# Kernel tuning notes

Hardware: AMD Instinct MI355X
Metric: run time of the kernel (lower is better)

Reference implementation:

```python
import jax, jax.numpy as jnp
import numpy as np

NUM_GRAPHS = 1024  # number of graphs in the batch (readout segments)


def setup_inputs() -> dict:
    key = jax.random.key(0)
    ks = jax.random.split(key, 10)
    N, F_IN, F1, F2, E = 100000, 64, 128, 64, 3200000
    x = jax.random.normal(ks[0], (N, F_IN), dtype=jnp.float32)
    adj = jax.random.randint(ks[1], (2, E), 0, N, dtype=jnp.int64)
    batch = jnp.sort(jax.random.randint(ks[2], (N,), 0, NUM_GRAPHS, dtype=jnp.int64))
    def xavier(k, shape):
        fan_in, fan_out = shape
        lim = jnp.sqrt(6.0 / (fan_in + fan_out))
        return jax.random.uniform(k, shape, jnp.float32, -lim, lim)
    W1 = xavier(ks[3], (F_IN, F1)); b1 = jax.random.uniform(ks[4], (F1,), jnp.float32)
    W2 = xavier(ks[5], (F1, F2));  b2 = jax.random.uniform(ks[6], (F2,), jnp.float32)
    Wm = xavier(ks[7], (2 * F2, F2)); bm = jax.random.uniform(ks[8], (F2,), jnp.float32)
    return {"x": x, "adj": adj, "batch": batch,
            "W1": W1, "b1": b1, "W2": W2, "b2": b2, "Wm": Wm, "bm": bm}


def _gcn_conv(x, W, b, src, dst):
    # GCNConv: out = D^{-1/2} (A + I) D^{-1/2} X W + b
    N = x.shape[0]
    h = x @ W  # [N, F_out]
    loops = jnp.arange(N, dtype=src.dtype)
    src_a = jnp.concatenate([src, loops])  # add self-loops
    dst_a = jnp.concatenate([dst, loops])
    deg = jax.ops.segment_sum(jnp.ones(src_a.shape[0], h.dtype), dst_a, num_segments=N)
    dinv = jax.lax.rsqrt(deg)  # deg >= 1 due to self-loops
    norm = dinv[src_a] * dinv[dst_a]  # [E+N]
    msg = h[src_a] * norm[:, None]    # gather + scale (memory-bound)
    return jax.ops.segment_sum(msg, dst_a, num_segments=N) + b


def _readout_meanmax(x, batch):
    G = NUM_GRAPHS
    s = jax.ops.segment_sum(x, batch, num_segments=G)
    cnt = jax.ops.segment_sum(jnp.ones(x.shape[0], x.dtype), batch, num_segments=G)
    mean = s / jnp.maximum(cnt, 1.0)[:, None]
    mx = jax.ops.segment_max(x, batch, num_segments=G)
    return jnp.concatenate([mean, mx], axis=1)  # [G, 2*F2]


def reference(x, adj, batch, W1, b1, W2, b2, Wm, bm):
    src, dst = adj[0], adj[1]
    h = jax.nn.relu(_gcn_conv(x, W1, b1, src, dst))
    h = _gcn_conv(h, W2, b2, src, dst)
    r = _readout_meanmax(h, batch)
    return r @ Wm + bm
```

## Files before the change

kernel.cpp:

```cpp
#include <hip/hip_runtime.h>
#include <hip/hip_fp16.h>
#include <cstdint>
#include <cstddef>

#define NGRAPH 1024
#define CHUNK 8192
#define SCTHREADS 512
#define SCIT (CHUNK / SCTHREADS)
#define MAXB 512
#define CAP 16384

typedef _Float16 f16x8 __attribute__((ext_vector_type(8)));
typedef float f32x4 __attribute__((ext_vector_type(4)));


__global__ __launch_bounds__(SCTHREADS) void scatter1_kernel(const int* __restrict__ src,
        const int* __restrict__ dst, int E, int B,
        int* __restrict__ bcnt, unsigned* __restrict__ ebuck) {
    __shared__ unsigned sorted[CHUNK];
    __shared__ int h[MAXB];
    __shared__ int lo[MAXB];
    __shared__ int cur[MAXB];
    __shared__ int gbase[MAXB];
    int blk = blockIdx.x, tid = threadIdx.x;
    int base = blk * CHUNK;
    int cnt_i = E - base; if (cnt_i > CHUNK) cnt_i = CHUNK;

    h[tid] = 0;
    __syncthreads();

    unsigned rd[SCIT], rs[SCIT];
    #pragma unroll
    for (int it = 0; it < SCIT; ++it) {
        int i = base + tid + it * SCTHREADS;
        if (i < E) {
            rd[it] = (unsigned)dst[i];
            rs[it] = (unsigned)src[i];
            atomicAdd(&h[rd[it] >> 8], 1);
        } else rd[it] = 0xFFFFFFFFu;
    }
    __syncthreads();

    int hv = h[tid];
    if (tid < B) gbase[tid] = hv ? atomicAdd(&bcnt[tid], hv) : 0;

    for (int o = 1; o < SCTHREADS; o <<= 1) {
        int t = (tid >= o) ? h[tid - o] : 0;
        __syncthreads();
        h[tid] += t;
        __syncthreads();
    }
    int excl = h[tid] - hv;
    lo[tid] = excl;
    cur[tid] = excl;
    __syncthreads();

    #pragma unroll
    for (int it = 0; it < SCIT; ++it) {
        if (rd[it] != 0xFFFFFFFFu) {
            int b = rd[it] >> 8;
            int p = atomicAdd(&cur[b], 1);
            sorted[p] = ((rd[it] & 255u) << 24) | rs[it];
        }
    }
    __syncthreads();

    for (int j = tid; j < cnt_i; j += SCTHREADS) {
        int l = (int)(((long long)j * B) / cnt_i);
        if (l > B - 1) l = B - 1;
        while (lo[l] > j) --l;
        while (l + 1 < B && lo[l + 1] <= j) ++l;
        ebuck[(size_t)l * CAP + gbase[l] + (j - lo[l])] = sorted[j];
    }
}

__global__ __launch_bounds__(256) void fine_kernel(const unsigned* __restrict__ ebuck,
        const int* __restrict__ bcnt, const float* __restrict__ x, int N, int B,
        int* __restrict__ row_beg, int* __restrict__ row_end, float* __restrict__ dinv,
        int* __restrict__ esrc, __half* __restrict__ xs) {
    __shared__ int hcnt[256];
    __shared__ int sc[256];
    __shared__ int loff[256];
    __shared__ float sdinv[256];
    int b = blockIdx.x, tid = threadIdx.x;
    int beg = b * CAP;
    int cnt = bcnt[b];
    hcnt[tid] = 0;
    __syncthreads();
    for (int e = tid; e < cnt; e += 256)
        atomicAdd(&hcnt[ebuck[beg + e] >> 24], 1);
    __syncthreads();
    int v = hcnt[tid];
    sc[tid] = v; __syncthreads();
    for (int o = 1; o < 256; o <<= 1) {
        int t = (tid >= o) ? sc[tid - o] : 0;
        __syncthreads();
        sc[tid] += t;
        __syncthreads();
    }
    int excl = sc[tid] - v;
    int n = (b << 8) + tid;
    float d = rsqrtf((float)(v + 1));
    if (n < N) {
        row_beg[n] = beg + excl;
        row_end[n] = beg + excl + v;
        dinv[n] = d;
    }
    loff[tid] = excl;
    sdinv[tid] = d;
    __syncthreads();
    for (int e = tid; e < cnt; e += 256) {
        unsigned u = ebuck[beg + e];
        int p = atomicAdd(&loff[u >> 24], 1);
        esrc[beg + p] = (int)(u & 0xFFFFFF);
    }
    const float4* xr = (const float4*)x;
    #pragma unroll
    for (int it = 0; it < 16; ++it) {
        int j = tid + it * 256;
        int node = j >> 4, cc = j & 15;
        int gn = (b << 8) + node;
        if (gn < N) {
            float dd = sdinv[node];
            float4 vv = xr[(size_t)gn * 16 + cc];
            __half2 h0 = __floats2half2_rn(vv.x * dd, vv.y * dd);
            __half2 h1 = __floats2half2_rn(vv.z * dd, vv.w * dd);
            uint2 u;
            u.x = *(unsigned*)&h0;
            u.y = *(unsigned*)&h1;
            ((uint2*)xs)[(size_t)gn * 16 + cc] = u;
        }
    }
}

__global__ __launch_bounds__(256) void prep_kernel(const float* __restrict__ W1,
        const float* __restrict__ W2, __half* __restrict__ W1s, __half* __restrict__ W2s,
        const int* __restrict__ batch, int N, int* __restrict__ goff,
        int* __restrict__ bcnt) {
    int t = threadIdx.x;
    if (blockIdx.x == 0) {
        #pragma unroll
        for (int it = 0; it < 4; ++it) {
            int s = t + it * 256;
            int n = s & 15, q = (s >> 4) & 3, nt = (s >> 6) & 7, ks = s >> 9;
            int k0 = ks * 32 + q * 8, col = nt * 16 + n;
            __align__(16) __half h[8];
            #pragma unroll
            for (int j = 0; j < 8; ++j) h[j] = (__half)W1[(k0 + j) * 128 + col];
            *((uint4*)&W1s[(size_t)s * 8]) = *(uint4*)h;
        }
        #pragma unroll
        for (int it = 0; it < 4; ++it) {
            int s = t + it * 256;
            int n = s & 15, q = (s >> 4) & 3, n2 = (s >> 6) & 3, ks2 = s >> 8;
            int k0 = ks2 * 32 + q * 8, col = n2 * 16 + n;
            __align__(16) __half h[8];
            #pragma unroll
            for (int j = 0; j < 8; ++j) h[j] = (__half)W2[(k0 + j) * 64 + col];
            *((uint4*)&W2s[(size_t)s * 8]) = *(uint4*)h;
        }
    } else {
        int g = (blockIdx.x - 1) * 256 + t;
        if (g < MAXB) bcnt[g] = 0;
        if (g > NGRAPH) return;
        if (g == NGRAPH) { goff[g] = N; return; }
        int lo = 0, hi = N;
        while (lo < hi) {
            int mid = (lo + hi) >> 1;
            if (batch[mid] < g) lo = mid + 1; else hi = mid;
        }
        goff[g] = lo;
    }
}

__device__ inline void acc8h(__half2* a, const uint4& u) {
    const __half2* h = (const __half2*)&u;
    #pragma unroll
    for (int i = 0; i < 4; ++i) a[i] = __hadd2(a[i], h[i]);
}

__global__ __launch_bounds__(256) void agg_h2h_kernel(const __half* __restrict__ xs,
        const int* __restrict__ esrc, const int* __restrict__ row_beg,
        const int* __restrict__ row_end, const float* __restrict__ dinv,
        __half* __restrict__ out, int N) {
    int n = blockIdx.x * 4 + (threadIdx.x >> 6);
    if (n >= N) return;
    int lane = threadIdx.x & 63;
    int g = lane >> 3, c = lane & 7;
    const uint4* xs4 = (const uint4*)xs;
    int beg = row_beg[n], end = row_end[n];
    __half2 ha[4] = {}, hb[4] = {};
    if (g == 0) acc8h(ha, xs4[(size_t)n * 8 + c]);
    int e = beg + g;
    for (; e + 8 < end; e += 16) {
        int s0 = esrc[e], s1 = esrc[e + 8];
        uint4 u0 = xs4[(size_t)s0 * 8 + c];
        uint4 u1 = xs4[(size_t)s1 * 8 + c];
        acc8h(ha, u0);
        acc8h(hb, u1);
    }
    if (e < end) acc8h(ha, xs4[(size_t)esrc[e] * 8 + c]);
    float a[8];
    #pragma unroll
    for (int i = 0; i < 4; ++i) {
        float2 fa = __half22float2(ha[i]), fb = __half22float2(hb[i]);
        a[2 * i]     = fa.x + fb.x;
        a[2 * i + 1] = fa.y + fb.y;
    }
    #pragma unroll
    for (int i = 0; i < 8; ++i) {
        a[i] += __shfl_xor(a[i], 8, 64);
        a[i] += __shfl_xor(a[i], 16, 64);
        a[i] += __shfl_xor(a[i], 32, 64);
    }
    if (g == 0) {
        float d = dinv[n];
        __align__(16) __half2 h[4];
        #pragma unroll
        for (int i = 0; i < 4; ++i)
            h[i] = __floats2half2_rn(a[2 * i] * d, a[2 * i + 1] * d);
        ((uint4*)out)[(size_t)n * 8 + c] = *(uint4*)h;
    }
}

__global__ __launch_bounds__(256) void agg_h2f_kernel(const __half* __restrict__ xs,
        const int* __restrict__ esrc, const int* __restrict__ row_beg,
        const int* __restrict__ row_end, const float* __restrict__ dinv,
        const float* __restrict__ bias, float* __restrict__ out, int N) {
    int n = blockIdx.x * 4 + (threadIdx.x >> 6);
    if (n >= N) return;
    int lane = threadIdx.x & 63;
    int g = lane >> 3, c = lane & 7;
    const uint4* xs4 = (const uint4*)xs;
    int beg = row_beg[n], end = row_end[n];
    __half2 ha[4] = {}, hb[4] = {};
    if (g == 0) acc8h(ha, xs4[(size_t)n * 8 + c]);
    int e = beg + g;
    for (; e + 8 < end; e += 16) {
        int s0 = esrc[e], s1 = esrc[e + 8];
        uint4 u0 = xs4[(size_t)s0 * 8 + c];
        uint4 u1 = xs4[(size_t)s1 * 8 + c];
        acc8h(ha, u0);
        acc8h(hb, u1);
    }
    if (e < end) acc8h(ha, xs4[(size_t)esrc[e] * 8 + c]);
    float a[8];
    #pragma unroll
    for (int i = 0; i < 4; ++i) {
        float2 fa = __half22float2(ha[i]), fb = __half22float2(hb[i]);
        a[2 * i]     = fa.x + fb.x;
        a[2 * i + 1] = fa.y + fb.y;
    }
    #pragma unroll
    for (int i = 0; i < 8; ++i) {
        a[i] += __shfl_xor(a[i], 8, 64);
        a[i] += __shfl_xor(a[i], 16, 64);
        a[i] += __shfl_xor(a[i], 32, 64);
    }
    if (g == 0) {
        float d = dinv[n];
        float4 bb0 = ((const float4*)bias)[c * 2];
        float4 bb1 = ((const float4*)bias)[c * 2 + 1];
        float4 o0, o1;
        o0.x = a[0] * d + bb0.x; o0.y = a[1] * d + bb0.y;
        o0.z = a[2] * d + bb0.z; o0.w = a[3] * d + bb0.w;
        o1.x = a[4] * d + bb1.x; o1.y = a[5] * d + bb1.y;
        o1.z = a[6] * d + bb1.z; o1.w = a[7] * d + bb1.w;
        ((float4*)out)[(size_t)n * 16 + c * 2] = o0;
        ((float4*)out)[(size_t)n * 16 + c * 2 + 1] = o1;
    }
}

__global__ __launch_bounds__(256) void fusedmlp_kernel(const __half* __restrict__ A,
        const __half* __restrict__ W1s, const __half* __restrict__ W2s,
        const float* __restrict__ b1, const float* __restrict__ dinv,
        __half* __restrict__ T, int N) {
    __shared__ __align__(16) __half h1t[4][16][136];
    int tid = threadIdx.x;
    int w = tid >> 6, lane = tid & 63;
    int n15 = lane & 15, q = lane >> 4;
    int base = blockIdx.x * 64 + w * 16;

    int m = base + n15; if (m >= N) m = N - 1;
    const uint4* Ar = (const uint4*)(A + (size_t)m * 64);
    uint4 ua0 = Ar[q];
    uint4 ua1 = Ar[4 + q];
    f16x8 a10 = *(f16x8*)&ua0;
    f16x8 a11 = *(f16x8*)&ua1;
    const uint4* W1f = (const uint4*)W1s;
    #pragma unroll
    for (int nt = 0; nt < 8; ++nt) {
        f32x4 c = {0.f, 0.f, 0.f, 0.f};
        uint4 ub0 = W1f[(nt * 4 + q) * 16 + n15];
        uint4 ub1 = W1f[((8 + nt) * 4 + q) * 16 + n15];
        c = __builtin_amdgcn_mfma_f32_16x16x32_f16(a10, *(f16x8*)&ub0, c, 0, 0, 0);
        c = __builtin_amdgcn_mfma_f32_16x16x32_f16(a11, *(f16x8*)&ub1, c, 0, 0, 0);
        float bv = b1[nt * 16 + n15];
        #pragma unroll
        for (int rr = 0; rr < 4; ++rr) {
            float hv = fmaxf(c[rr] + bv, 0.f);
            h1t[w][q * 4 + rr][nt * 16 + n15] = (__half)hv;
        }
    }
    __syncthreads();

    f16x8 a2[4];
    #pragma unroll
    for (int ks2 = 0; ks2 < 4; ++ks2)
        a2[ks2] = *(f16x8*)&h1t[w][n15][ks2 * 32 + q * 8];
    const uint4* W2f = (const uint4*)W2s;
    #pragma unroll
    for (int n2 = 0; n2 < 4; ++n2) {
        f32x4 c = {0.f, 0.f, 0.f, 0.f};
        #pragma unroll
        for (int ks2 = 0; ks2 < 4; ++ks2) {
            uint4 ub = W2f[((ks2 * 4 + n2) * 4 + q) * 16 + n15];
            c = __builtin_amdgcn_mfma_f32_16x16x32_f16(a2[ks2], *(f16x8*)&ub, c, 0, 0, 0);
        }
        #pragma unroll
        for (int rr = 0; rr < 4; ++rr) {
            int node = base + q * 4 + rr;
            if (node < N) {
                float v = c[rr] * dinv[node];
                T[(size_t)node * 64 + n2 * 16 + n15] = (__half)v;
            }
        }
    }
}

__global__ __launch_bounds__(256) void readout_head_kernel(const float* __restrict__ h2,
        const int* __restrict__ goff, const float* __restrict__ Wm,
        const float* __restrict__ bm, float* __restrict__ out) {
    int g = blockIdx.x;
    int beg = goff[g], end = goff[g + 1];
    int f = threadIdx.x & 63;
    int c = threadIdx.x >> 6;
    float s = 0.f, m = -3.4e38f;
    for (int n = beg + c; n < end; n += 4) {
        float v = h2[(size_t)n * 64 + f];
        s += v;
        m = fmaxf(m, v);
    }
    __shared__ float ss[4][64], sm[4][64];
    __shared__ float rr[128];
    ss[c][f] = s; sm[c][f] = m;
    __syncthreads();
    if (c == 0) {
        float S = ss[0][f] + ss[1][f] + ss[2][f] + ss[3][f];
        float M = fmaxf(fmaxf(sm[0][f], sm[1][f]), fmaxf(sm[2][f], sm[3][f]));
        int cnt = end - beg;
        rr[f] = (cnt > 0) ? S / (float)cnt : 0.f;
        rr[64 + f] = (cnt > 0) ? M : 0.f;
    }
    __syncthreads();
    if (threadIdx.x < 64) {
        int j = threadIdx.x;
        float acc = bm[j];
        #pragma unroll 4
        for (int k = 0; k < 128; ++k)
            acc = fmaf(rr[k], Wm[k * 64 + j], acc);
        out[(size_t)g * 64 + j] = acc;
    }
}

extern "C" void kernel_launch(void* const* d_in, const int* in_sizes, int n_in,
                              void* d_out, int out_size, void* d_ws, size_t ws_size,
                              hipStream_t stream) {
    const float* x    = (const float*)d_in[0];
    const int*  adj   = (const int*)d_in[1];
    const int*  batch = (const int*)d_in[2];
    const float* W1   = (const float*)d_in[3];
    const float* b1   = (const float*)d_in[4];
    const float* W2   = (const float*)d_in[5];
    const float* b2   = (const float*)d_in[6];
    const float* Wm   = (const float*)d_in[7];
    const float* bm   = (const float*)d_in[8];
    float* out = (float*)d_out;

    const int N = in_sizes[0] / 64;
    const int E = in_sizes[1] / 2;
    const int* src = adj;
    const int* dst = adj + E;
    const int B = (N + 255) >> 8;
    const int nblocks = (E + CHUNK - 1) / CHUNK;

    char* w = (char*)d_ws;
    size_t off = 0;
    auto carve = [&](size_t bytes) -> void* {
        void* p = w + off;
        off += (bytes + 255) & ~(size_t)255;
        return p;
    };
    size_t halfbuf = (size_t)N * 64 * 2;
    float* dinv    = (float*)carve((size_t)N * 4);
    int*   row_beg = (int*)  carve((size_t)N * 4);
    int*   row_end = (int*)  carve((size_t)N * 4);
    int*   esrc    = (int*)  carve((size_t)B * CAP * 4);
    unsigned* ebuck= (unsigned*)carve((size_t)B * CAP * 4);
    int*   bcnt    = (int*)  carve((MAXB + 1) * 4);
    int*   goff    = (int*)  carve((NGRAPH + 1) * 4);
    __half* W1s    = (__half*)carve(8192 * 2);
    __half* W2s    = (__half*)carve(8192 * 2);
    __half* xs_h   = (__half*)carve(halfbuf);
    __half* agg1h  = (__half*)carve(halfbuf);
    float* h2      = (float*)carve((size_t)N * 64 * 4);
    __half* ts_h = xs_h;

    prep_kernel<<<1 + (NGRAPH + 256) / 256, 256, 0, stream>>>(W1, W2, W1s, W2s,
                                                              batch, N, goff, bcnt);

    scatter1_kernel<<<nblocks, SCTHREADS, 0, stream>>>(src, dst, E, B, bcnt, ebuck);
    fine_kernel<<<B, 256, 0, stream>>>(ebuck, bcnt, x, N, B, row_beg, row_end,
                                       dinv, esrc, xs_h);

    agg_h2h_kernel<<<(N + 3) / 4, 256, 0, stream>>>(xs_h, esrc, row_beg, row_end,
                                                    dinv, agg1h, N);

    fusedmlp_kernel<<<(N + 63) / 64, 256, 0, stream>>>(agg1h, W1s, W2s, b1, dinv, ts_h, N);

    agg_h2f_kernel<<<(N + 3) / 4, 256, 0, stream>>>(ts_h, esrc, row_beg, row_end,
                                                    dinv, b2, h2, N);

    readout_head_kernel<<<NGRAPH, 256, 0, stream>>>(h2, goff, Wm, bm, out);
}
```

Before: 309.6 us.

## Fuse first-layer aggregation into the MLP kernel via shared-memory tiles

Merges the layer-1 neighbor aggregation kernel with the fused two-matmul MFMA kernel. Each wave now aggregates its 16 nodes one after another into an LDS tile, then runs both matmuls from LDS. This removes the intermediate fp16 buffer round trip and one launch. The cost is less parallelism in the gather phase: 16x fewer blocks, and each wave loops serially over 16 nodes. It also adds extra LDS use, which may lower occupancy.

```diff
diff --git a/kernel.cpp b/kernel.cpp
--- a/kernel.cpp
+++ b/kernel.cpp
@@ -179,47 +179,102 @@
     for (int i = 0; i < 4; ++i) a[i] = __hadd2(a[i], h[i]);
 }
 
-__global__ __launch_bounds__(256) void agg_h2h_kernel(const __half* __restrict__ xs,
+__global__ __launch_bounds__(256) void agg_mlp_kernel(const __half* __restrict__ xs,
         const int* __restrict__ esrc, const int* __restrict__ row_beg,
         const int* __restrict__ row_end, const float* __restrict__ dinv,
-        __half* __restrict__ out, int N) {
-    int n = blockIdx.x * 4 + (threadIdx.x >> 6);
-    if (n >= N) return;
-    int lane = threadIdx.x & 63;
+        const __half* __restrict__ W1s, const __half* __restrict__ W2s,
+        const float* __restrict__ b1, __half* __restrict__ T, int N) {
+    __shared__ __align__(16) __half aggt[4][16][136];
+    __shared__ __align__(16) __half h1t[4][16][136];
+    int tid = threadIdx.x;
+    int w = tid >> 6, lane = tid & 63;
     int g = lane >> 3, c = lane & 7;
+    int n15 = lane & 15, q = lane >> 4;
+    int base = blockIdx.x * 64 + w * 16;
     const uint4* xs4 = (const uint4*)xs;
-    int beg = row_beg[n], end = row_end[n];
-    __half2 ha[4] = {}, hb[4] = {};
-    if (g == 0) acc8h(ha, xs4[(size_t)n * 8 + c]);
-    int e = beg + g;
-    for (; e + 8 < end; e += 16) {
-        int s0 = esrc[e], s1 = esrc[e + 8];
-        uint4 u0 = xs4[(size_t)s0 * 8 + c];
-        uint4 u1 = xs4[(size_t)s1 * 8 + c];
-        acc8h(ha, u0);
-        acc8h(hb, u1);
-    }
-    if (e < end) acc8h(ha, xs4[(size_t)esrc[e] * 8 + c]);
-    float a[8];
-    #pragma unroll
-    for (int i = 0; i < 4; ++i) {
-        float2 fa = __half22float2(ha[i]), fb = __half22float2(hb[i]);
-        a[2 * i]     = fa.x + fb.x;
-        a[2 * i + 1] = fa.y + fb.y;
-    }
-    #pragma unroll
-    for (int i = 0; i < 8; ++i) {
-        a[i] += __shfl_xor(a[i], 8, 64);
-        a[i] += __shfl_xor(a[i], 16, 64);
-        a[i] += __shfl_xor(a[i], 32, 64);
-    }
-    if (g == 0) {
-        float d = dinv[n];
-        __align__(16) __half2 h[4];
-        #pragma unroll
-        for (int i = 0; i < 4; ++i)
-            h[i] = __floats2half2_rn(a[2 * i] * d, a[2 * i + 1] * d);
-        ((uint4*)out)[(size_t)n * 8 + c] = *(uint4*)h;
+
+    for (int j = 0; j < 16; ++j) {
+        int n = base + j;
+        if (n >= N) {
+            if (g == 0) *((uint4*)&aggt[w][j][c * 8]) = make_uint4(0, 0, 0, 0);
+            continue;
+        }
+        int beg = row_beg[n], end = row_end[n];
+        __half2 ha[4] = {}, hb[4] = {};
+        if (g == 0) acc8h(ha, xs4[(size_t)n * 8 + c]);
+        int e = beg + g;
+        for (; e + 8 < end; e += 16) {
+            int s0 = esrc[e], s1 = esrc[e + 8];
+            uint4 u0 = xs4[(size_t)s0 * 8 + c];
+            uint4 u1 = xs4[(size_t)s1 * 8 + c];
+            acc8h(ha, u0);
+            acc8h(hb, u1);
+        }
+        if (e < end) acc8h(ha, xs4[(size_t)esrc[e] * 8 + c]);
+        float a[8];
+        #pragma unroll
+        for (int i = 0; i < 4; ++i) {
+            float2 fa = __half22float2(ha[i]), fb = __half22float2(hb[i]);
+            a[2 * i]     = fa.x + fb.x;
+            a[2 * i + 1] = fa.y + fb.y;
+        }
+        #pragma unroll
+        for (int i = 0; i < 8; ++i) {
+            a[i] += __shfl_xor(a[i], 8, 64);
+            a[i] += __shfl_xor(a[i], 16, 64);
+            a[i] += __shfl_xor(a[i], 32, 64);
+        }
+        if (g == 0) {
+            float d = dinv[n];
+            __align__(16) __half2 h[4];
+            #pragma unroll
+            for (int i = 0; i < 4; ++i)
+                h[i] = __floats2half2_rn(a[2 * i] * d, a[2 * i + 1] * d);
+            *((uint4*)&aggt[w][j][c * 8]) = *(uint4*)h;
+        }
+    }
+    __syncthreads();
+
+    f16x8 a10 = *(f16x8*)&aggt[w][n15][q * 8];
+    f16x8 a11 = *(f16x8*)&aggt[w][n15][32 + q * 8];
+    const uint4* W1f = (const uint4*)W1s;
+    #pragma unroll
+    for (int nt = 0; nt < 8; ++nt) {
+        f32x4 cc = {0.f, 0.f, 0.f, 0.f};
+        uint4 ub0 = W1f[(nt * 4 + q) * 16 + n15];
+        uint4 ub1 = W1f[((8 + nt) * 4 + q) * 16 + n15];
+        cc = __builtin_amdgcn_mfma_f32_16x16x32_f16(a10, *(f16x8*)&ub0, cc, 0, 0, 0);
+        cc = __builtin_amdgcn_mfma_f32_16x16x32_f16(a11, *(f16x8*)&ub1, cc, 0, 0, 0);
+        float bv = b1[nt * 16 + n15];
+        #pragma unroll
+        for (int rr = 0; rr < 4; ++rr) {
+            float hv = fmaxf(cc[rr] + bv, 0.f);
+            h1t[w][q * 4 + rr][nt * 16 + n15] = (__half)hv;
+        }
+    }
+    __syncthreads();
+
+    f16x8 a2[4];
+    #pragma unroll
+    for (int ks2 = 0; ks2 < 4; ++ks2)
+        a2[ks2] = *(f16x8*)&h1t[w][n15][ks2 * 32 + q * 8];
+    const uint4* W2f = (const uint4*)W2s;
+    #pragma unroll
+    for (int n2 = 0; n2 < 4; ++n2) {
+        f32x4 cc = {0.f, 0.f, 0.f, 0.f};
+        #pragma unroll
+        for (int ks2 = 0; ks2 < 4; ++ks2) {
+            uint4 ub = W2f[((ks2 * 4 + n2) * 4 + q) * 16 + n15];
+            cc = __builtin_amdgcn_mfma_f32_16x16x32_f16(a2[ks2], *(f16x8*)&ub, cc, 0, 0, 0);
+        }
+        #pragma unroll
+        for (int rr = 0; rr < 4; ++rr) {
+            int node = base + q * 4 + rr;
+            if (node < N) {
+                float v = cc[rr] * dinv[node];
+                T[(size_t)node * 64 + n2 * 16 + n15] = (__half)v;
+            }
+        }
     }
 }
 
@@ -271,63 +326,6 @@
     }
 }
 
-__global__ __launch_bounds__(256) void fusedmlp_kernel(const __half* __restrict__ A,
-        const __half* __restrict__ W1s, const __half* __restrict__ W2s,
-        const float* __restrict__ b1, const float* __restrict__ dinv,
-        __half* __restrict__ T, int N) {
-    __shared__ __align__(16) __half h1t[4][16][136];
-    int tid = threadIdx.x;
-    int w = tid >> 6, lane = tid & 63;
-    int n15 = lane & 15, q = lane >> 4;
-    int base = blockIdx.x * 64 + w * 16;
-
-    int m = base + n15; if (m >= N) m = N - 1;
-    const uint4* Ar = (const uint4*)(A + (size_t)m * 64);
-    uint4 ua0 = Ar[q];
-    uint4 ua1 = Ar[4 + q];
-    f16x8 a10 = *(f16x8*)&ua0;
-    f16x8 a11 = *(f16x8*)&ua1;
-    const uint4* W1f = (const uint4*)W1s;
-    #pragma unroll
-    for (int nt = 0; nt < 8; ++nt) {
-        f32x4 c = {0.f, 0.f, 0.f, 0.f};
-        uint4 ub0 = W1f[(nt * 4 + q) * 16 + n15];
-        uint4 ub1 = W1f[((8 + nt) * 4 + q) * 16 + n15];
-        c = __builtin_amdgcn_mfma_f32_16x16x32_f16(a10, *(f16x8*)&ub0, c, 0, 0, 0);
-        c = __builtin_amdgcn_mfma_f32_16x16x32_f16(a11, *(f16x8*)&ub1, c, 0, 0, 0);
-        float bv = b1[nt * 16 + n15];
-        #pragma unroll
-        for (int rr = 0; rr < 4; ++rr) {
-            float hv = fmaxf(c[rr] + bv, 0.f);
-            h1t[w][q * 4 + rr][nt * 16 + n15] = (__half)hv;
-        }
-    }
-    __syncthreads();
-
-    f16x8 a2[4];
-    #pragma unroll
-    for (int ks2 = 0; ks2 < 4; ++ks2)
-        a2[ks2] = *(f16x8*)&h1t[w][n15][ks2 * 32 + q * 8];
-    const uint4* W2f = (const uint4*)W2s;
-    #pragma unroll
-    for (int n2 = 0; n2 < 4; ++n2) {
-        f32x4 c = {0.f, 0.f, 0.f, 0.f};
-        #pragma unroll
-        for (int ks2 = 0; ks2 < 4; ++ks2) {
-            uint4 ub = W2f[((ks2 * 4 + n2) * 4 + q) * 16 + n15];
-            c = __builtin_amdgcn_mfma_f32_16x16x32_f16(a2[ks2], *(f16x8*)&ub, c, 0, 0, 0);
-        }
-        #pragma unroll
-        for (int rr = 0; rr < 4; ++rr) {
-            int node = base + q * 4 + rr;
-            if (node < N) {
-                float v = c[rr] * dinv[node];
-                T[(size_t)node * 64 + n2 * 16 + n15] = (__half)v;
-            }
-        }
-    }
-}
-
 __global__ __launch_bounds__(256) void readout_head_kernel(const float* __restrict__ h2,
         const int* __restrict__ goff, const float* __restrict__ Wm,
         const float* __restrict__ bm, float* __restrict__ out) {
@@ -402,9 +400,8 @@
     __half* W1s    = (__half*)carve(8192 * 2);
     __half* W2s    = (__half*)carve(8192 * 2);
     __half* xs_h   = (__half*)carve(halfbuf);
-    __half* agg1h  = (__half*)carve(halfbuf);
+    __half* ts_h   = (__half*)carve(halfbuf);
     float* h2      = (float*)carve((size_t)N * 64 * 4);
-    __half* ts_h = xs_h;
 
     prep_kernel<<<1 + (NGRAPH + 256) / 256, 256, 0, stream>>>(W1, W2, W1s, W2s,
                                                               batch, N, goff, bcnt);
@@ -413,10 +410,8 @@
     fine_kernel<<<B, 256, 0, stream>>>(ebuck, bcnt, x, N, B, row_beg, row_end,
                                        dinv, esrc, xs_h);
 
-    agg_h2h_kernel<<<(N + 3) / 4, 256, 0, stream>>>(xs_h, esrc, row_beg, row_end,
-                                                    dinv, agg1h, N);
-
-    fusedmlp_kernel<<<(N + 63) / 64, 256, 0, stream>>>(agg1h, W1s, W2s, b1, dinv, ts_h, N);
+    agg_mlp_kernel<<<(N + 63) / 64, 256, 0, stream>>>(xs_h, esrc, row_beg, row_end,
+                                                      dinv, W1s, W2s, b1, ts_h, N);
 
     agg_h2f_kernel<<<(N + 3) / 4, 256, 0, stream>>>(ts_h, esrc, row_beg, row_end,
                                                     dinv, b2, h2, N);
```

Measured after the change: 344.2 us. +11.2%, slower.
